# Optimization experiments

Hardware: AMD Instinct MI355X
Metric: run time of the kernel (lower is better)

Reference implementation:

```python
import jax, jax.numpy as jnp
import numpy as np

N_NODES = 50000
NEG_SLOPE = 0.2  # PyG GATConv default leaky_relu slope


def gat_conv(x, src, dst, W, a_src, a_dst, b, heads, out_ch, concat):
    """PyG-style GATConv. src/dst: [E] edge endpoints (messages flow src->dst)."""
    n = N_NODES
    h = (x @ W).reshape(n, heads, out_ch)            # [N, H, C]
    # per-node attention logits, gathered per edge
    s_src = (h * a_src).sum(-1)                       # [N, H]
    s_dst = (h * a_dst).sum(-1)                       # [N, H]
    e = jax.nn.leaky_relu(s_src[src] + s_dst[dst], NEG_SLOPE)  # [E, H]
    # segment softmax over incoming edges of each dst node
    e_max = jax.ops.segment_max(e, dst, num_segments=n)        # [N, H]
    ex = jnp.exp(e - e_max[dst])                                # [E, H]
    denom = jax.ops.segment_sum(ex, dst, num_segments=n)       # [N, H]
    alpha = ex / denom[dst]                                     # [E, H]
    # scatter-add weighted messages
    out = jax.ops.segment_sum(h[src] * alpha[:, :, None], dst, num_segments=n)  # [N, H, C]
    if concat:
        out = out.reshape(n, heads * out_ch)
    else:
        out = out.mean(axis=1)
    return out + b


def setup_inputs() -> dict:
    key = jax.random.key(0)
    ks = jax.random.split(key, 16)
    n, e = N_NODES, 400000
    in_ch, hidden, out_ch = 3, 64, 32
    x = jax.random.normal(ks[0], (n, in_ch), dtype=jnp.float32)
    edge_index = jax.random.randint(ks[1], (2, e), 0, n, dtype=jnp.int32)

    def glorot(k, shape):
        fan = sum(shape)
        return jax.random.uniform(k, shape, jnp.float32, -1.0, 1.0) * jnp.sqrt(6.0 / fan)

    # layer 1: in=3 -> hidden=64, heads=4, concat
    W1 = glorot(ks[2], (in_ch, 4 * hidden))
    a_src1 = glorot(ks[3], (4, hidden))
    a_dst1 = glorot(ks[4], (4, hidden))
    b1 = jnp.zeros((4 * hidden,), jnp.float32)
    # layer 2: 256 -> 64, heads=4, concat
    W2 = glorot(ks[5], (4 * hidden, 4 * hidden))
    a_src2 = glorot(ks[6], (4, hidden))
    a_dst2 = glorot(ks[7], (4, hidden))
    b2 = jnp.zeros((4 * hidden,), jnp.float32)
    # layer 3: 256 -> 32, heads=1, mean (concat=False)
    W3 = glorot(ks[8], (4 * hidden, out_ch))
    a_src3 = glorot(ks[9], (1, out_ch))
    a_dst3 = glorot(ks[10], (1, out_ch))
    b3 = jnp.zeros((out_ch,), jnp.float32)
    return dict(x=x, edge_index=edge_index,
                W1=W1, a_src1=a_src1, a_dst1=a_dst1, b1=b1,
                W2=W2, a_src2=a_src2, a_dst2=a_dst2, b2=b2,
                W3=W3, a_src3=a_src3, a_dst3=a_dst3, b3=b3)


def reference(x, edge_index,
              W1, a_src1, a_dst1, b1,
              W2, a_src2, a_dst2, b2,
              W3, a_src3, a_dst3, b3):
    n = N_NODES
    loops = jnp.arange(n, dtype=edge_index.dtype)
    src = jnp.concatenate([edge_index[0], loops])  # PyG adds self-loops by default
    dst = jnp.concatenate([edge_index[1], loops])
    h = gat_conv(x, src, dst, W1, a_src1, a_dst1, b1, heads=4, out_ch=64, concat=True)
    h = jax.nn.relu(h)  # dropout is identity in eval mode
    h = gat_conv(h, src, dst, W2, a_src2, a_dst2, b2, heads=4, out_ch=64, concat=True)
    h = jax.nn.relu(h)
    out = gat_conv(h, src, dst, W3, a_src3, a_dst3, b3, heads=1, out_ch=32, concat=False)
    return out
```

## Files before the change

### kernel.cpp

```cpp
#include <hip/hip_runtime.h>
#include <math.h>


#define NEG_SLOPE 0.2f
#define CAP 40

typedef unsigned short u16;
typedef unsigned int u32;
typedef short bf16x8 __attribute__((ext_vector_type(8)));
typedef float floatx4 __attribute__((ext_vector_type(4)));

__device__ __forceinline__ float b2f(u16 u) {
    return __uint_as_float(((unsigned int)u) << 16);
}
__device__ __forceinline__ u16 f2b(float f) {
    unsigned int u = __float_as_uint(f);
    unsigned int r = (u + 0x7fffu + ((u >> 16) & 1u)) >> 16;
    return (u16)r;
}
__device__ __forceinline__ void load16(const u16* g, u16* l) {
    __builtin_amdgcn_global_load_lds(
        (const __attribute__((address_space(1))) void*)g,
        (__attribute__((address_space(3))) void*)l, 16, 0, 0);
}


__device__ __forceinline__ void pack_dev(const float* __restrict__ W,
                                         u16* __restrict__ Bhi,
                                         u16* __restrict__ Blo, int N, int idx) {
    int CT = N / 16;
    int lane = idx & 63;
    int ctkb = idx >> 6;
    int ct = ctkb % CT;
    int kb = ctkb / CT;
    int col = ct * 16 + (lane & 15);
    int k0 = kb * 32 + (lane >> 4) * 8;
#pragma unroll
    for (int j = 0; j < 8; ++j) {
        float w = W[(size_t)(k0 + j) * N + col];
        u16 hi = f2b(w);
        Bhi[(size_t)idx * 8 + j] = hi;
        Blo[(size_t)idx * 8 + j] = f2b(w - b2f(hi));
    }
}


__global__ __launch_bounds__(256) void fill_prep(
    const int* __restrict__ ei,
    const float* __restrict__ W1, const float* __restrict__ as1,
    const float* __restrict__ ad1,
    const float* __restrict__ W2, const float* __restrict__ W3,
    u16* __restrict__ B2h, u16* __restrict__ B2l,
    u16* __restrict__ B3h, u16* __restrict__ B3l,
    float* __restrict__ vsd, int* __restrict__ cursor,
    int* __restrict__ csr, int n, int E) {
    const int tid = threadIdx.x;
    const int tg = blockIdx.x * 256 + tid;
    const int NTH = gridDim.x * 256;
    const int Etot = E + n;
    const int lane = tid & 63;

    if (tg < 8192) {
        pack_dev(W2, B2h, B2l, 256, tg);
    } else if (tg < 9216) {
        pack_dev(W3, B3h, B3l, 32, tg - 8192);
    } else if (tg < 9472) {
        int j = tg - 9216;
        float a_s = as1[j], a_d = ad1[j];
#pragma unroll
        for (int k = 0; k < 3; ++k) {
            float w = W1[k * 256 + j];
            float ps = w * a_s, pd = w * a_d;
#pragma unroll
            for (int o = 32; o > 0; o >>= 1) {
                ps += __shfl_xor(ps, o);
                pd += __shfl_xor(pd, o);
            }
            if (lane == 0) {
                vsd[(j >> 6) * 3 + k] = ps;
                vsd[12 + (j >> 6) * 3 + k] = pd;
            }
        }
    }
    for (int e = tg; e < Etot; e += NTH) {
        int src, dst;
        if (e < E) { src = ei[e]; dst = ei[E + e]; }
        else       { src = e - E; dst = e - E; }
        int old = atomicAdd(&cursor[dst], 1);
        if (old < CAP) csr[dst * CAP + old] = src;
    }
}


__global__ __launch_bounds__(256) void gat_aggregate_l1(const float* __restrict__ x,
                                                        const float* __restrict__ vsd,
                                                        const int* __restrict__ cur,
                                                        const int* __restrict__ csr,
                                                        const float* __restrict__ W1,
                                                        const float* __restrict__ bias,
                                                        u16* __restrict__ outHi, int n) {
    int node = blockIdx.x * 4 + (threadIdx.x >> 6);
    int lane = threadIdx.x & 63;
    if (node >= n) return;
    const int hB = lane & 3;
    const int eL = lane >> 2;
    const int hA = lane >> 4;
    int beg = node * CAP;
    int end = beg + min(cur[node], CAP);

    float vs0 = vsd[hB * 3 + 0], vs1 = vsd[hB * 3 + 1], vs2 = vsd[hB * 3 + 2];
    float vd0 = vsd[12 + hB * 3 + 0], vd1 = vsd[12 + hB * 3 + 1], vd2 = vsd[12 + hB * 3 + 2];
    float xd0 = x[node * 3 + 0], xd1 = x[node * 3 + 1], xd2 = x[node * 3 + 2];
    float sd = fmaf(xd0, vd0, fmaf(xd1, vd1, xd2 * vd2));

    float m = -INFINITY, l = 0.f;
    float ax = 0.f, ay = 0.f, az = 0.f;

    for (int base = beg; base < end; base += 16) {
        int j = base + eL;
        bool valid = (j < end);
        int sj = valid ? csr[j] : 0;
        float x0 = x[sj * 3 + 0];
        float x1 = x[sj * 3 + 1];
        float x2 = x[sj * 3 + 2];
        float logit = -INFINITY;
        if (valid) {
            float xv = fmaf(x0, vs0, fmaf(x1, vs1, x2 * vs2)) + sd;
            logit = (xv > 0.f) ? xv : NEG_SLOPE * xv;
        }
        float cm = logit;
        cm = fmaxf(cm, __shfl_xor(cm, 4));
        cm = fmaxf(cm, __shfl_xor(cm, 8));
        cm = fmaxf(cm, __shfl_xor(cm, 16));
        cm = fmaxf(cm, __shfl_xor(cm, 32));
        float nm = fmaxf(m, cm);
        float scale = __expf(m - nm);
        float ex = valid ? __expf(logit - nm) : 0.f;
        float es = ex;
        es += __shfl_xor(es, 4);
        es += __shfl_xor(es, 8);
        es += __shfl_xor(es, 16);
        es += __shfl_xor(es, 32);
        l = l * scale + es;
        m = nm;
        float sA = __shfl(scale, hA);
        ax *= sA; ay *= sA; az *= sA;

        int cnt = min(16, end - base);
        for (int t = 0; t < cnt; ++t) {
            float a  = __shfl(ex, t * 4 + hA);
            float bx = __shfl(x0, t * 4);
            float by = __shfl(x1, t * 4);
            float bz = __shfl(x2, t * 4);
            ax = fmaf(a, bx, ax);
            ay = fmaf(a, by, ay);
            az = fmaf(a, bz, az);
        }
    }

    float lf = __shfl(l, hA);
    float inv = 1.f / lf;
    ax *= inv; ay *= inv; az *= inv;

    int c = lane * 4;
    const float4 w0 = *(const float4*)&W1[0 * 256 + c];
    const float4 w1 = *(const float4*)&W1[1 * 256 + c];
    const float4 w2 = *(const float4*)&W1[2 * 256 + c];
    const float4 bv = *(const float4*)&bias[c];
    float4 o;
    o.x = fmaxf(fmaf(ax, w0.x, fmaf(ay, w1.x, fmaf(az, w2.x, bv.x))), 0.f);
    o.y = fmaxf(fmaf(ax, w0.y, fmaf(ay, w1.y, fmaf(az, w2.y, bv.y))), 0.f);
    o.z = fmaxf(fmaf(ax, w0.z, fmaf(ay, w1.z, fmaf(az, w2.z, bv.z))), 0.f);
    o.w = fmaxf(fmaf(ax, w0.w, fmaf(ay, w1.w, fmaf(az, w2.w, bv.w))), 0.f);
    ushort4 h4;
    h4.x = f2b(o.x);
    h4.y = f2b(o.y);
    h4.z = f2b(o.z);
    h4.w = f2b(o.w);
    *(ushort4*)&outHi[(size_t)node * 256 + c] = h4;
}


template <int CT, int HEADS>
__global__ __launch_bounds__(512, 4) void gemm_async(const u16* __restrict__ Ahi,
                                                     const u16* __restrict__ Bhi,
                                                     const u16* __restrict__ Blo,
                                                     const float* __restrict__ asrc,
                                                     const float* __restrict__ adst,
                                                     u16* __restrict__ Hb,
                                                     float* __restrict__ ssrc,
                                                     float* __restrict__ sdst, int n) {
    constexpr int THREADS = 512;
    constexpr int BFRAG = CT * 64;
    constexpr int BSZ = BFRAG * 8;
    __shared__ __align__(16) u16 lds[2][2 * BSZ];

    int t = threadIdx.x;
    int w = t >> 6, l = t & 63;
    int m0 = blockIdx.x * 128 + w * 16;
    int lm = l & 15, q = l >> 4;

    int arow = min(m0 + lm, n - 1);
    const u16* aH = Ahi + (size_t)arow * 256 + q * 8;

    floatx4 acc[CT] = {};

    auto stageB = [&](int buf, int kb) {
        u16* L = &lds[buf][0];
        constexpr int BROUNDS = (BFRAG + THREADS - 1) / THREADS;
#pragma unroll
        for (int r = 0; r < BROUNDS; ++r) {
            int u = r * THREADS + t;
            if ((BFRAG % THREADS == 0) || u < BFRAG) {
                size_t off = ((size_t)kb * BFRAG + (size_t)u) * 8;
                u16* Lb = L + (size_t)(r * THREADS + w * 64) * 8;
                load16(Bhi + off, Lb);
                load16(Blo + off, Lb + BSZ);
            }
        }
    };

    stageB(0, 0);
    bf16x8 ahi = *(const bf16x8*)aH;
    __syncthreads();

    for (int kb = 0; kb < 8; ++kb) {
        int cur = kb & 1;
        bf16x8 nhi = ahi;
        if (kb < 7) {
            stageB(cur ^ 1, kb + 1);
            nhi = *(const bf16x8*)(aH + (kb + 1) * 32);
        }
        const u16* L = &lds[cur][0];
#pragma unroll
        for (int ct = 0; ct < CT; ++ct) {
            bf16x8 bhi = *(const bf16x8*)&L[(ct * 64 + l) * 8];
            bf16x8 blo = *(const bf16x8*)&L[BSZ + (ct * 64 + l) * 8];
            acc[ct] = __builtin_amdgcn_mfma_f32_16x16x32_bf16(ahi, bhi, acc[ct], 0, 0, 0);
            acc[ct] = __builtin_amdgcn_mfma_f32_16x16x32_bf16(ahi, blo, acc[ct], 0, 0, 0);
        }
        __syncthreads();
        ahi = nhi;
    }

#pragma unroll
    for (int ct = 0; ct < CT; ++ct) {
#pragma unroll
        for (int r = 0; r < 4; ++r) {
            int row = m0 + q * 4 + r;
            if (row < n)
                Hb[(size_t)row * (CT * 16) + ct * 16 + lm] = f2b(acc[ct][r]);
        }
    }
    constexpr int CPH = CT / HEADS;
    float ps[4][HEADS] = {}, pd[4][HEADS] = {};
#pragma unroll
    for (int h = 0; h < HEADS; ++h) {
#pragma unroll
        for (int j = 0; j < CPH; ++j) {
            int ct = h * CPH + j;
            float a_s = asrc[ct * 16 + lm];
            float a_d = adst[ct * 16 + lm];
#pragma unroll
            for (int r = 0; r < 4; ++r) {
                ps[r][h] = fmaf(acc[ct][r], a_s, ps[r][h]);
                pd[r][h] = fmaf(acc[ct][r], a_d, pd[r][h]);
            }
        }
    }
#pragma unroll
    for (int r = 0; r < 4; ++r)
#pragma unroll
        for (int h = 0; h < HEADS; ++h)
#pragma unroll
            for (int o = 1; o < 16; o <<= 1) {
                ps[r][h] += __shfl_xor(ps[r][h], o);
                pd[r][h] += __shfl_xor(pd[r][h], o);
            }
#pragma unroll
    for (int h = 0; h < HEADS; ++h) {
        if (lm == h) {
#pragma unroll
            for (int r = 0; r < 4; ++r) {
                int row = m0 + q * 4 + r;
                if (row < n) {
                    ssrc[row * HEADS + h] = ps[r][h];
                    sdst[row * HEADS + h] = pd[r][h];
                }
            }
        }
    }
}


__global__ __launch_bounds__(256, 4) void agg_m4_g3(
    const u16* __restrict__ Hb,
    const float* __restrict__ ssrc, const float* __restrict__ sdst,
    const int* __restrict__ cur, const int* __restrict__ csr,
    const float* __restrict__ bias2,
    const u16* __restrict__ B3h, const u16* __restrict__ B3l,
    const float* __restrict__ as3, const float* __restrict__ ad3,
    u16* __restrict__ Hb3, float* __restrict__ ssrc3,
    float* __restrict__ sdst3, int n) {
    constexpr int BSZ3 = 8 * 2 * 64 * 8;
    __shared__ __align__(16) u16 sB[2 * BSZ3];

    const int t = threadIdx.x;
    const int w = t >> 6;
    const int lane = t & 63;
    const int m0 = blockIdx.x * 64 + w * 16;
    const int lm = lane & 15, q = lane >> 4;

#pragma unroll
    for (int r = 0; r < 4; ++r) {
        int u = r * 256 + t;
        u16* Ldst = sB + (size_t)(r * 256 + w * 64) * 8;
        load16(B3h + (size_t)u * 8, Ldst);
        load16(B3l + (size_t)u * 8, Ldst + BSZ3);
    }

    const int hB = lane & 3;
    const int eL = lane >> 2;
    const int hA = lane >> 4;
    const float4 bv = *(const float4*)&bias2[lane * 4];

    bf16x8 abuf[8];
    for (int i = 0; i < 16; ++i) {
        int node = m0 + i;
        float4 o = make_float4(0.f, 0.f, 0.f, 0.f);
        if (node < n) {
            int beg = node * CAP;
            int end = beg + min(cur[node], CAP);
            float sd = sdst[node * 4 + hB];
            float m = -INFINITY, l = 0.f;
            float4 acc4 = make_float4(0.f, 0.f, 0.f, 0.f);

            for (int base = beg; base < end; base += 16) {
                int j = base + eL;
                bool valid = (j < end);
                int sj = valid ? csr[j] : 0;
                float logit = -INFINITY;
                if (valid) {
                    float xv = ssrc[sj * 4 + hB] + sd;
                    logit = (xv > 0.f) ? xv : NEG_SLOPE * xv;
                }
                float cm = logit;
                cm = fmaxf(cm, __shfl_xor(cm, 4));
                cm = fmaxf(cm, __shfl_xor(cm, 8));
                cm = fmaxf(cm, __shfl_xor(cm, 16));
                cm = fmaxf(cm, __shfl_xor(cm, 32));
                float nm = fmaxf(m, cm);
                float scale = __expf(m - nm);
                float ex = valid ? __expf(logit - nm) : 0.f;
                float es = ex;
                es += __shfl_xor(es, 4);
                es += __shfl_xor(es, 8);
                es += __shfl_xor(es, 16);
                es += __shfl_xor(es, 32);
                l = l * scale + es;
                m = nm;
                float sA = __shfl(scale, hA);
                acc4.x *= sA; acc4.y *= sA; acc4.z *= sA; acc4.w *= sA;

                int cnt = min(16, end - base);
                for (int tt = 0; tt < cnt; tt += 4) {
#pragma unroll
                    for (int u = 0; u < 4; ++u) {
                        int e = tt + u;
                        float a = __shfl(ex, e * 4 + hA);
                        int s = __shfl(sj, e * 4);
                        ushort4 hv = *(const ushort4*)&Hb[(size_t)s * 256 + lane * 4];
                        acc4.x = fmaf(a, b2f(hv.x), acc4.x);
                        acc4.y = fmaf(a, b2f(hv.y), acc4.y);
                        acc4.z = fmaf(a, b2f(hv.z), acc4.z);
                        acc4.w = fmaf(a, b2f(hv.w), acc4.w);
                    }
                }
            }
            float lf = __shfl(l, hA);
            float inv = 1.f / lf;
            o.x = fmaxf(fmaf(acc4.x, inv, bv.x), 0.f);
            o.y = fmaxf(fmaf(acc4.y, inv, bv.y), 0.f);
            o.z = fmaxf(fmaf(acc4.z, inv, bv.z), 0.f);
            o.w = fmaxf(fmaf(acc4.w, inv, bv.w), 0.f);
        }
        u32 p0 = ((u32)f2b(o.y) << 16) | f2b(o.x);
        u32 p1 = ((u32)f2b(o.w) << 16) | f2b(o.z);
#pragma unroll
        for (int kb = 0; kb < 8; ++kb) {
            int s0 = kb * 8 + q * 2;
            u32 a0 = __shfl(p0, s0);
            u32 a1 = __shfl(p1, s0);
            u32 a2 = __shfl(p0, s0 + 1);
            u32 a3 = __shfl(p1, s0 + 1);
            if (lm == i) {
                union { uint4 u4; bf16x8 v; } cv;
                cv.u4 = make_uint4(a0, a1, a2, a3);
                abuf[kb] = cv.v;
            }
        }
    }

    __syncthreads();

    floatx4 acc[2] = {};
#pragma unroll
    for (int kb = 0; kb < 8; ++kb) {
#pragma unroll
        for (int ct = 0; ct < 2; ++ct) {
            const u16* base = sB + (size_t)((kb * 2 + ct) * 64 + lane) * 8;
            bf16x8 bhi = *(const bf16x8*)base;
            bf16x8 blo = *(const bf16x8*)(base + BSZ3);
            acc[ct] = __builtin_amdgcn_mfma_f32_16x16x32_bf16(abuf[kb], bhi, acc[ct], 0, 0, 0);
            acc[ct] = __builtin_amdgcn_mfma_f32_16x16x32_bf16(abuf[kb], blo, acc[ct], 0, 0, 0);
        }
    }

#pragma unroll
    for (int ct = 0; ct < 2; ++ct) {
#pragma unroll
        for (int r = 0; r < 4; ++r) {
            int row = m0 + q * 4 + r;
            if (row < n)
                Hb3[(size_t)row * 32 + ct * 16 + lm] = f2b(acc[ct][r]);
        }
    }
    float ps[4] = {}, pd[4] = {};
#pragma unroll
    for (int ct = 0; ct < 2; ++ct) {
        float a_s = as3[ct * 16 + lm];
        float a_d = ad3[ct * 16 + lm];
#pragma unroll
        for (int r = 0; r < 4; ++r) {
            ps[r] = fmaf(acc[ct][r], a_s, ps[r]);
            pd[r] = fmaf(acc[ct][r], a_d, pd[r]);
        }
    }
#pragma unroll
    for (int r = 0; r < 4; ++r)
#pragma unroll
        for (int o = 1; o < 16; o <<= 1) {
            ps[r] += __shfl_xor(ps[r], o);
            pd[r] += __shfl_xor(pd[r], o);
        }
    if (lm == 0) {
#pragma unroll
        for (int r = 0; r < 4; ++r) {
            int row = m0 + q * 4 + r;
            if (row < n) { ssrc3[row] = ps[r]; sdst3[row] = pd[r]; }
        }
    }
}


__global__ __launch_bounds__(256) void gat_aggregate_h1(const u16* __restrict__ Hb,
                                                        const float* __restrict__ ssrc,
                                                        const float* __restrict__ sdst,
                                                        const int* __restrict__ cur,
                                                        const int* __restrict__ csr,
                                                        const float* __restrict__ bias,
                                                        float* __restrict__ out, int n) {
    int node = blockIdx.x * 4 + (threadIdx.x >> 6);
    int lane = threadIdx.x & 63;
    if (node >= n) return;
    int dg = min(cur[node], CAP);
    int beg = node * CAP;
    float sd = sdst[node];

    bool valid = (lane < dg);
    int sj = valid ? csr[beg + lane] : 0;
    float logit = -INFINITY;
    if (valid) {
        float xv = ssrc[sj] + sd;
        logit = (xv > 0.f) ? xv : NEG_SLOPE * xv;
    }
    float cm = logit;
#pragma unroll
    for (int o = 32; o > 0; o >>= 1) cm = fmaxf(cm, __shfl_xor(cm, o));
    float ex = valid ? __expf(logit - cm) : 0.f;
    float l = ex;
#pragma unroll
    for (int o = 32; o > 0; o >>= 1) l += __shfl_xor(l, o);

    const int eh = lane >> 5;
    const int ch = lane & 31;
    float acc = 0.f;
    for (int t = 0; t < dg; t += 8) {
#pragma unroll
        for (int u = 0; u < 4; ++u) {
            int e = t + u * 2 + eh;
            float a = __shfl(ex, e & 63);
            int s = __shfl(sj, e & 63);
            if (e < dg) acc = fmaf(a, b2f(Hb[(size_t)s * 32 + ch]), acc);
        }
    }
    acc += __shfl_xor(acc, 32);
    if (lane < 32) out[(size_t)node * 32 + lane] = acc / l + bias[lane];
}


extern "C" void kernel_launch(void* const* d_in, const int* in_sizes, int n_in,
                              void* d_out, int out_size, void* d_ws, size_t ws_size,
                              hipStream_t stream) {
    const float* x   = (const float*)d_in[0];
    const int*   ei  = (const int*)d_in[1];
    const float* W1  = (const float*)d_in[2];
    const float* as1 = (const float*)d_in[3];
    const float* ad1 = (const float*)d_in[4];
    const float* b1  = (const float*)d_in[5];
    const float* W2  = (const float*)d_in[6];
    const float* as2 = (const float*)d_in[7];
    const float* ad2 = (const float*)d_in[8];
    const float* b2  = (const float*)d_in[9];
    const float* W3  = (const float*)d_in[10];
    const float* as3 = (const float*)d_in[11];
    const float* ad3 = (const float*)d_in[12];
    const float* b3  = (const float*)d_in[13];
    float* out = (float*)d_out;

    const int n = in_sizes[0] / 3;
    const int E = in_sizes[1] / 2;
    const int Etot = E + n;

    char* ws = (char*)d_ws;
    u16* Fhi  = (u16*)ws;    ws += (size_t)n * 256 * sizeof(u16);
    u16* Hb   = (u16*)ws;    ws += (size_t)n * 256 * sizeof(u16);
    u16* Hb3  = (u16*)ws;    ws += (size_t)n * 32 * sizeof(u16);
    u16* B2h  = (u16*)ws;    ws += (size_t)8 * 16 * 64 * 8 * sizeof(u16);
    u16* B2l  = (u16*)ws;    ws += (size_t)8 * 16 * 64 * 8 * sizeof(u16);
    u16* B3h  = (u16*)ws;    ws += (size_t)8 * 2 * 64 * 8 * sizeof(u16);
    u16* B3l  = (u16*)ws;    ws += (size_t)8 * 2 * 64 * 8 * sizeof(u16);
    float* ssrc = (float*)ws;  ws += (size_t)n * 4 * sizeof(float);
    float* sdst = (float*)ws;  ws += (size_t)n * 4 * sizeof(float);
    float* ssrc3 = (float*)ws; ws += (size_t)n * sizeof(float);
    float* sdst3 = (float*)ws; ws += (size_t)n * sizeof(float);
    float* vsd  = (float*)ws;  ws += 32 * sizeof(float);
    int* cursor = (int*)ws;    ws += (size_t)n * sizeof(int);
    int* csr    = (int*)ws;    ws += (size_t)n * CAP * sizeof(int);

    hipMemsetAsync(cursor, 0, (size_t)n * sizeof(int), stream);

    int eblocks = (Etot + 255) / 256;
    int nb4 = (n + 3) / 4;
    int nb64 = (n + 63) / 64;
    int nb128 = (n + 127) / 128;

    fill_prep<<<eblocks, 256, 0, stream>>>(ei, W1, as1, ad1, W2, W3,
                                           B2h, B2l, B3h, B3l, vsd,
                                           cursor, csr, n, E);

    gat_aggregate_l1<<<nb4, 256, 0, stream>>>(x, vsd, cursor, csr, W1, b1,
                                              Fhi, n);

    gemm_async<16, 4><<<nb128, 512, 0, stream>>>(Fhi, B2h, B2l, as2, ad2,
                                                 Hb, ssrc, sdst, n);

    agg_m4_g3<<<nb64, 256, 0, stream>>>(Hb, ssrc, sdst, cursor, csr, b2,
                                        B3h, B3l, as3, ad3,
                                        Hb3, ssrc3, sdst3, n);

    gat_aggregate_h1<<<nb4, 256, 0, stream>>>(Hb3, ssrc3, sdst3, cursor, csr,
                                              b3, out, n);
}
```

Measured before the change: 249.2 us.

## Assign one wavefront per node in fused layer-2 aggregation plus layer-3 GEMM

Result: faster. 233.0 us (-6.5%).

```diff
diff --git a/kernel.cpp b/kernel.cpp
--- a/kernel.cpp
+++ b/kernel.cpp
@@ -4,6 +4,7 @@
 
 #define NEG_SLOPE 0.2f
 #define CAP 40
+#define FROW 264
 
 typedef unsigned short u16;
 typedef unsigned int u32;
@@ -293,7 +294,7 @@
 }
 
 
-__global__ __launch_bounds__(256, 4) void agg_m4_g3(
+__global__ __launch_bounds__(1024, 2) void agg_m4_g3(
     const u16* __restrict__ Hb,
     const float* __restrict__ ssrc, const float* __restrict__ sdst,
     const int* __restrict__ cur, const int* __restrict__ csr,
@@ -304,19 +305,23 @@
     float* __restrict__ sdst3, int n) {
     constexpr int BSZ3 = 8 * 2 * 64 * 8;
     __shared__ __align__(16) u16 sB[2 * BSZ3];
+    __shared__ __align__(16) u16 sF[16 * FROW];
 
     const int t = threadIdx.x;
     const int w = t >> 6;
     const int lane = t & 63;
-    const int m0 = blockIdx.x * 64 + w * 16;
-    const int lm = lane & 15, q = lane >> 4;
-
-#pragma unroll
-    for (int r = 0; r < 4; ++r) {
-        int u = r * 256 + t;
-        u16* Ldst = sB + (size_t)(r * 256 + w * 64) * 8;
+    const int m0 = blockIdx.x * 16;
+    const int node = m0 + w;
+
+    {
+        int u = t;
+        u16* Ldst = sB + (size_t)(w * 64) * 8;
         load16(B3h + (size_t)u * 8, Ldst);
         load16(B3l + (size_t)u * 8, Ldst + BSZ3);
+        int u2 = t + 1024;
+        u16* Ldst2 = sB + (size_t)(1024 + w * 64) * 8;
+        load16(B3h + (size_t)u2 * 8, Ldst2);
+        load16(B3l + (size_t)u2 * 8, Ldst2 + BSZ3);
     }
 
     const int hB = lane & 3;
@@ -324,130 +329,118 @@
     const int hA = lane >> 4;
     const float4 bv = *(const float4*)&bias2[lane * 4];
 
-    bf16x8 abuf[8];
-    for (int i = 0; i < 16; ++i) {
-        int node = m0 + i;
-        float4 o = make_float4(0.f, 0.f, 0.f, 0.f);
-        if (node < n) {
-            int beg = node * CAP;
-            int end = beg + min(cur[node], CAP);
-            float sd = sdst[node * 4 + hB];
-            float m = -INFINITY, l = 0.f;
-            float4 acc4 = make_float4(0.f, 0.f, 0.f, 0.f);
-
-            for (int base = beg; base < end; base += 16) {
-                int j = base + eL;
-                bool valid = (j < end);
-                int sj = valid ? csr[j] : 0;
-                float logit = -INFINITY;
-                if (valid) {
-                    float xv = ssrc[sj * 4 + hB] + sd;
-                    logit = (xv > 0.f) ? xv : NEG_SLOPE * xv;
+    float4 o = make_float4(0.f, 0.f, 0.f, 0.f);
+    if (node < n) {
+        int beg = node * CAP;
+        int end = beg + min(cur[node], CAP);
+        float sd = sdst[node * 4 + hB];
+        float m = -INFINITY, l = 0.f;
+        float4 acc4 = make_float4(0.f, 0.f, 0.f, 0.f);
+
+        for (int base = beg; base < end; base += 16) {
+            int j = base + eL;
+            bool valid = (j < end);
+            int sj = valid ? csr[j] : 0;
+            float logit = -INFINITY;
+            if (valid) {
+                float xv = ssrc[sj * 4 + hB] + sd;
+                logit = (xv > 0.f) ? xv : NEG_SLOPE * xv;
+            }
+            float cm = logit;
+            cm = fmaxf(cm, __shfl_xor(cm, 4));
+            cm = fmaxf(cm, __shfl_xor(cm, 8));
+            cm = fmaxf(cm, __shfl_xor(cm, 16));
+            cm = fmaxf(cm, __shfl_xor(cm, 32));
+            float nm = fmaxf(m, cm);
+            float scale = __expf(m - nm);
+            float ex = valid ? __expf(logit - nm) : 0.f;
+            float es = ex;
+            es += __shfl_xor(es, 4);
+            es += __shfl_xor(es, 8);
+            es += __shfl_xor(es, 16);
+            es += __shfl_xor(es, 32);
+            l = l * scale + es;
+            m = nm;
+            float sA = __shfl(scale, hA);
+            acc4.x *= sA; acc4.y *= sA; acc4.z *= sA; acc4.w *= sA;
+
+            int cnt = min(16, end - base);
+            for (int tt = 0; tt < cnt; tt += 4) {
+#pragma unroll
+                for (int u = 0; u < 4; ++u) {
+                    int e = tt + u;
+                    float a = __shfl(ex, e * 4 + hA);
+                    int s = __shfl(sj, e * 4);
+                    ushort4 hv = *(const ushort4*)&Hb[(size_t)s * 256 + lane * 4];
+                    acc4.x = fmaf(a, b2f(hv.x), acc4.x);
+                    acc4.y = fmaf(a, b2f(hv.y), acc4.y);
+                    acc4.z = fmaf(a, b2f(hv.z), acc4.z);
+                    acc4.w = fmaf(a, b2f(hv.w), acc4.w);
                 }
-                float cm = logit;
-                cm = fmaxf(cm, __shfl_xor(cm, 4));
-                cm = fmaxf(cm, __shfl_xor(cm, 8));
-                cm = fmaxf(cm, __shfl_xor(cm, 16));
-                cm = fmaxf(cm, __shfl_xor(cm, 32));
-                float nm = fmaxf(m, cm);
-                float scale = __expf(m - nm);
-                float ex = valid ? __expf(logit - nm) : 0.f;
-                float es = ex;
-                es += __shfl_xor(es, 4);
-                es += __shfl_xor(es, 8);
-                es += __shfl_xor(es, 16);
-                es += __shfl_xor(es, 32);
-                l = l * scale + es;
-                m = nm;
-                float sA = __shfl(scale, hA);
-                acc4.x *= sA; acc4.y *= sA; acc4.z *= sA; acc4.w *= sA;
-
-                int cnt = min(16, end - base);
-                for (int tt = 0; tt < cnt; tt += 4) {
-#pragma unroll
-                    for (int u = 0; u < 4; ++u) {
-                        int e = tt + u;
-                        float a = __shfl(ex, e * 4 + hA);
-                        int s = __shfl(sj, e * 4);
-                        ushort4 hv = *(const ushort4*)&Hb[(size_t)s * 256 + lane * 4];
-                        acc4.x = fmaf(a, b2f(hv.x), acc4.x);
-                        acc4.y = fmaf(a, b2f(hv.y), acc4.y);
-                        acc4.z = fmaf(a, b2f(hv.z), acc4.z);
-                        acc4.w = fmaf(a, b2f(hv.w), acc4.w);
-                    }
-                }
-            }
-            float lf = __shfl(l, hA);
-            float inv = 1.f / lf;
-            o.x = fmaxf(fmaf(acc4.x, inv, bv.x), 0.f);
-            o.y = fmaxf(fmaf(acc4.y, inv, bv.y), 0.f);
-            o.z = fmaxf(fmaf(acc4.z, inv, bv.z), 0.f);
-            o.w = fmaxf(fmaf(acc4.w, inv, bv.w), 0.f);
-        }
-        u32 p0 = ((u32)f2b(o.y) << 16) | f2b(o.x);
-        u32 p1 = ((u32)f2b(o.w) << 16) | f2b(o.z);
+            }
+        }
+        float lf = __shfl(l, hA);
+        float inv = 1.f / lf;
+        o.x = fmaxf(fmaf(acc4.x, inv, bv.x), 0.f);
+        o.y = fmaxf(fmaf(acc4.y, inv, bv.y), 0.f);
+        o.z = fmaxf(fmaf(acc4.z, inv, bv.z), 0.f);
+        o.w = fmaxf(fmaf(acc4.w, inv, bv.w), 0.f);
+    }
+    u32 p0 = ((u32)f2b(o.y) << 16) | f2b(o.x);
+    u32 p1 = ((u32)f2b(o.w) << 16) | f2b(o.z);
+    *(u32*)&sF[w * FROW + lane * 4]     = p0;
+    *(u32*)&sF[w * FROW + lane * 4 + 2] = p1;
+
+    __syncthreads();
+
+    if (w == 0) {
+        const int lm = lane & 15, q = lane >> 4;
+        floatx4 acc[2] = {};
 #pragma unroll
         for (int kb = 0; kb < 8; ++kb) {
-            int s0 = kb * 8 + q * 2;
-            u32 a0 = __shfl(p0, s0);
-            u32 a1 = __shfl(p1, s0);
-            u32 a2 = __shfl(p0, s0 + 1);
-            u32 a3 = __shfl(p1, s0 + 1);
-            if (lm == i) {
-                union { uint4 u4; bf16x8 v; } cv;
-                cv.u4 = make_uint4(a0, a1, a2, a3);
-                abuf[kb] = cv.v;
-            }
-        }
-    }
-
-    __syncthreads();
-
-    floatx4 acc[2] = {};
-#pragma unroll
-    for (int kb = 0; kb < 8; ++kb) {
+            bf16x8 af = *(const bf16x8*)&sF[lm * FROW + kb * 32 + q * 8];
+#pragma unroll
+            for (int ct = 0; ct < 2; ++ct) {
+                const u16* base = sB + (size_t)((kb * 2 + ct) * 64 + lane) * 8;
+                bf16x8 bhi = *(const bf16x8*)base;
+                bf16x8 blo = *(const bf16x8*)(base + BSZ3);
+                acc[ct] = __builtin_amdgcn_mfma_f32_16x16x32_bf16(af, bhi, acc[ct], 0, 0, 0);
+                acc[ct] = __builtin_amdgcn_mfma_f32_16x16x32_bf16(af, blo, acc[ct], 0, 0, 0);
+            }
+        }
 #pragma unroll
         for (int ct = 0; ct < 2; ++ct) {
-            const u16* base = sB + (size_t)((kb * 2 + ct) * 64 + lane) * 8;
-            bf16x8 bhi = *(const bf16x8*)base;
-            bf16x8 blo = *(const bf16x8*)(base + BSZ3);
-            acc[ct] = __builtin_amdgcn_mfma_f32_16x16x32_bf16(abuf[kb], bhi, acc[ct], 0, 0, 0);
-            acc[ct] = __builtin_amdgcn_mfma_f32_16x16x32_bf16(abuf[kb], blo, acc[ct], 0, 0, 0);
-        }
-    }
-
-#pragma unroll
-    for (int ct = 0; ct < 2; ++ct) {
-#pragma unroll
-        for (int r = 0; r < 4; ++r) {
-            int row = m0 + q * 4 + r;
-            if (row < n)
-                Hb3[(size_t)row * 32 + ct * 16 + lm] = f2b(acc[ct][r]);
-        }
-    }
-    float ps[4] = {}, pd[4] = {};
-#pragma unroll
-    for (int ct = 0; ct < 2; ++ct) {
-        float a_s = as3[ct * 16 + lm];
-        float a_d = ad3[ct * 16 + lm];
-#pragma unroll
-        for (int r = 0; r < 4; ++r) {
-            ps[r] = fmaf(acc[ct][r], a_s, ps[r]);
-            pd[r] = fmaf(acc[ct][r], a_d, pd[r]);
-        }
-    }
-#pragma unroll
-    for (int r = 0; r < 4; ++r)
-#pragma unroll
-        for (int o = 1; o < 16; o <<= 1) {
-            ps[r] += __shfl_xor(ps[r], o);
-            pd[r] += __shfl_xor(pd[r], o);
-        }
-    if (lm == 0) {
-#pragma unroll
-        for (int r = 0; r < 4; ++r) {
-            int row = m0 + q * 4 + r;
-            if (row < n) { ssrc3[row] = ps[r]; sdst3[row] = pd[r]; }
+#pragma unroll
+            for (int r = 0; r < 4; ++r) {
+                int row = m0 + q * 4 + r;
+                if (row < n)
+                    Hb3[(size_t)row * 32 + ct * 16 + lm] = f2b(acc[ct][r]);
+            }
+        }
+        float ps[4] = {}, pd[4] = {};
+#pragma unroll
+        for (int ct = 0; ct < 2; ++ct) {
+            float a_s = as3[ct * 16 + lm];
+            float a_d = ad3[ct * 16 + lm];
+#pragma unroll
+            for (int r = 0; r < 4; ++r) {
+                ps[r] = fmaf(acc[ct][r], a_s, ps[r]);
+                pd[r] = fmaf(acc[ct][r], a_d, pd[r]);
+            }
+        }
+#pragma unroll
+        for (int r = 0; r < 4; ++r)
+#pragma unroll
+            for (int oo = 1; oo < 16; oo <<= 1) {
+                ps[r] += __shfl_xor(ps[r], oo);
+                pd[r] += __shfl_xor(pd[r], oo);
+            }
+        if (lm == 0) {
+#pragma unroll
+            for (int r = 0; r < 4; ++r) {
+                int row = m0 + q * 4 + r;
+                if (row < n) { ssrc3[row] = ps[r]; sdst3[row] = pd[r]; }
+            }
         }
     }
 }
@@ -542,7 +535,7 @@
 
     int eblocks = (Etot + 255) / 256;
     int nb4 = (n + 3) / 4;
-    int nb64 = (n + 63) / 64;
+    int nb16 = (n + 15) / 16;
     int nb128 = (n + 127) / 128;
 
     fill_prep<<<eblocks, 256, 0, stream>>>(ei, W1, as1, ad1, W2, W3,
@@ -555,9 +548,9 @@
     gemm_async<16, 4><<<nb128, 512, 0, stream>>>(Fhi, B2h, B2l, as2, ad2,
                                                  Hb, ssrc, sdst, n);
 
-    agg_m4_g3<<<nb64, 256, 0, stream>>>(Hb, ssrc, sdst, cursor, csr, b2,
-                                        B3h, B3l, as3, ad3,
-                                        Hb3, ssrc3, sdst3, n);
+    agg_m4_g3<<<nb16, 1024, 0, stream>>>(Hb, ssrc, sdst, cursor, csr, b2,
+                                         B3h, B3l, as3, ad3,
+                                         Hb3, ssrc3, sdst3, n);
 
     gat_aggregate_h1<<<nb4, 256, 0, stream>>>(Hb3, ssrc3, sdst3, cursor, csr,
                                               b3, out, n);
```
